# Optimization experiments

Measured on AMD Instinct MI355X. Metric: run time of the kernel, lower is better.

Reference implementation:

```python
import jax, jax.numpy as jnp
import numpy as np

NU, NI, E, NNZ, NLAYERS, TOPK = 2560, 3584, 64, 200000, 2, 5
N = NU + NI
DQK = 4 * E  # Linear(dim, 4*dim)


def setup_inputs() -> dict:
    key = jax.random.key(0)
    ks = jax.random.split(key, 14)
    s = 1.0 / np.sqrt(E)
    return {
        "user_emb": jax.random.normal(ks[0], (NU, E), jnp.float32) * s,
        "item_emb": jax.random.normal(ks[1], (NI, E), jnp.float32) * s,
        "norm_rows": jax.random.randint(ks[2], (NNZ,), 0, N, jnp.int32),
        "norm_cols": jax.random.randint(ks[3], (NNZ,), 0, N, jnp.int32),
        "norm_vals": jax.random.uniform(ks[4], (NNZ,), jnp.float32) / 32.0,
        "adj_rows": jax.random.randint(ks[5], (NNZ,), 0, N, jnp.int32),
        "adj_cols": jax.random.randint(ks[6], (NNZ,), 0, N, jnp.int32),
        "adj_vals": jnp.ones((NNZ,), jnp.float32),
        "Wq": jax.random.normal(ks[7], (DQK, E), jnp.float32) * s,
        "bq": jnp.zeros((DQK,), jnp.float32),
        "Wk": jax.random.normal(ks[8], (DQK, E), jnp.float32) * s,
        "bk": jnp.zeros((DQK,), jnp.float32),
        "Wv": jax.random.normal(ks[9], (DQK, E), jnp.float32) * s,
        "bv": jnp.zeros((DQK,), jnp.float32),
    }


def reference(user_emb, item_emb, norm_rows, norm_cols, norm_vals,
              adj_rows, adj_cols, adj_vals, Wq, bq, Wk, bk, Wv, bv):
    # densified sparse adjacencies (duplicates accumulated, as COO spmm would)
    A_norm = jnp.zeros((N, N), jnp.float32).at[norm_rows, norm_cols].add(norm_vals)
    A = jnp.zeros((N, N), jnp.float32).at[adj_rows, adj_cols].add(adj_vals)

    ego = jnp.concatenate([user_emb, item_emb], axis=0)  # [N, E]
    layers = []
    att_out = None
    for _ in range(NLAYERS):
        layers.append(ego)
        # GNN propagation: sparse.mm(norm_adj, ego)
        ego = A_norm @ ego  # [N, E]
        # dense similarity + sparse-blended similarity
        sim = ego @ ego.T                      # [N, N]
        sim = sim + 0.5 * (A @ sim)            # [N, N]
        # top-K neighbor selection + gather
        _, idx = jax.lax.top_k(sim, TOPK)      # [N, K]
        sample = ego[idx]                      # [N, K, E]
        # SampleAttention: Linear(dim, 4*dim) Q/K/V, scaled dot-product over K neighbors
        q = ego @ Wq.T + bq                    # [N, 4E]
        kk = sample @ Wk.T + bk                # [N, K, 4E]
        vv = sample @ Wv.T + bv                # [N, K, 4E]
        scores = jnp.einsum('nd,nkd->nk', q, kk) / jnp.sqrt(jnp.float32(DQK))
        att = jax.nn.softmax(scores, axis=-1)
        att_out = jnp.einsum('nk,nkd->nd', att, vv)  # [N, 4E]
    mean_emb = jnp.mean(jnp.stack(layers, axis=1), axis=1)  # [N, E]
    return mean_emb[:NU], mean_emb[NU:], att_out
```

## Files before the change

### kernel.cpp

```cpp
#include <hip/hip_runtime.h>
#include <hip/hip_bf16.h>
#include <math.h>

#define NUSER 2560
#define NITEM 3584
#define NN    6144
#define EDIM  64
#define NNZ   200000
#define DQK   256
#define KTOP  5
#define SPLITS 16
#define TPS    3
#define CK     8
#define ELLW   96
#define TPB   256
#define NBUILD 1563
#define BSTR  72

typedef __attribute__((ext_vector_type(8))) short bf16x8;
typedef __attribute__((ext_vector_type(4))) float f32x4;

__device__ __forceinline__ int pack2(float a, float b) {
    __hip_bfloat162 h = __float22bfloat162_rn(float2{a, b});
    return *(int*)&h;
}
__device__ __forceinline__ void ell_unpack(long long v, int* col, float* w) {
    *col = (int)(v & 0xffffffffLL);
    *w   = __int_as_float((int)(v >> 32));
}

__global__ void build_kernel(const int* __restrict__ nr, const int* __restrict__ nc,
                             const float* __restrict__ nv,
                             const int* __restrict__ ar, const int* __restrict__ ac,
                             const float* __restrict__ Wq, const float* __restrict__ Wk,
                             const float* __restrict__ bq,
                             int* __restrict__ cnt_n, int* __restrict__ cnt_a,
                             long long* __restrict__ cv_n, int* __restrict__ cv_a,
                             float* __restrict__ Gbuf) {
    int t = threadIdx.x;

    if (blockIdx.x >= NBUILD) {
        int gb = blockIdx.x - NBUILD;
        if (gb < 16) {
            int ei = gb * 4 + (t >> 6);
            int f  = t & 63;
            float a8[8];
#pragma unroll
            for (int u = 0; u < 8; ++u) a8[u] = 0.f;
            for (int d0 = 0; d0 < DQK; d0 += 8) {
#pragma unroll
                for (int u = 0; u < 8; ++u)
                    a8[u] = fmaf(Wq[(d0 + u) * 64 + ei], Wk[(d0 + u) * 64 + f], a8[u]);
            }
            Gbuf[ei * 64 + f] = ((a8[0] + a8[1]) + (a8[2] + a8[3]))
                              + ((a8[4] + a8[5]) + (a8[6] + a8[7]));
        } else {
            __shared__ float sm[256];
            int f = t & 63, dq = t >> 6;
            float p = 0.f;
            for (int d = dq * 64; d < dq * 64 + 64; ++d)
                p = fmaf(bq[d], Wk[d * 64 + f], p);
            sm[t] = p;
            __syncthreads();
            if (t < 64) Gbuf[4096 + t] = ((sm[t] + sm[64 + t]) + (sm[128 + t] + sm[192 + t]));
        }
        return;
    }

    int g = blockIdx.x * TPB + t;
    if (g < NNZ) {
        int r = nr[g], c = nc[g];
        float v = nv[g];
        int slot = atomicAdd(&cnt_n[r], 1);
        long long pk = (unsigned int)c | ((long long)(unsigned int)__float_as_int(v) << 32);
        cv_n[r * ELLW + slot] = pk;
    } else if (g < 2 * NNZ) {
        int h = g - NNZ;
        int r = ar[h], c = ac[h];
        int slot = atomicAdd(&cnt_a[r], 1);
        cv_a[r * ELLW + slot] = c;
    }
}

__global__ __launch_bounds__(TPB) void spmm_ell_emb_kernel(
        const int* __restrict__ cnt, const long long* __restrict__ cv,
        const float* __restrict__ user, const float* __restrict__ item,
        float* __restrict__ dst) {
    int r = blockIdx.x * 4 + (threadIdx.x >> 6);
    int lane = threadIdx.x & 63;
    int s = r * ELLW, e = s + cnt[r];
    float a[8];
#pragma unroll
    for (int u = 0; u < 8; ++u) a[u] = 0.f;
    int j = s, n8 = s + ((e - s) & ~7);
    for (; j < n8; j += 8) {
        int col[8]; float w[8];
#pragma unroll
        for (int u = 0; u < 8; ++u) ell_unpack(cv[j + u], &col[u], &w[u]);
#pragma unroll
        for (int u = 0; u < 8; ++u) {
            float x = (col[u] < NUSER) ? user[col[u] * EDIM + lane]
                                       : item[(col[u] - NUSER) * EDIM + lane];
            a[u] = fmaf(w[u], x, a[u]);
        }
    }
    for (; j < e; ++j) {
        int col; float w;
        ell_unpack(cv[j], &col, &w);
        float x = (col < NUSER) ? user[col * EDIM + lane] : item[(col - NUSER) * EDIM + lane];
        a[0] = fmaf(w, x, a[0]);
    }
    dst[r * EDIM + lane] = ((a[0] + a[1]) + (a[2] + a[3])) + ((a[4] + a[5]) + (a[6] + a[7]));
}

__global__ __launch_bounds__(TPB) void spmm_ell_kernel(
        const int* __restrict__ cnt, const long long* __restrict__ cv,
        const float* __restrict__ src, float* __restrict__ dst) {
    int r = blockIdx.x * 4 + (threadIdx.x >> 6);
    int lane = threadIdx.x & 63;
    int s = r * ELLW, e = s + cnt[r];
    float a[8];
#pragma unroll
    for (int u = 0; u < 8; ++u) a[u] = 0.f;
    int j = s, n8 = s + ((e - s) & ~7);
    for (; j < n8; j += 8) {
        int col[8]; float w[8];
#pragma unroll
        for (int u = 0; u < 8; ++u) ell_unpack(cv[j + u], &col[u], &w[u]);
#pragma unroll
        for (int u = 0; u < 8; ++u)
            a[u] = fmaf(w[u], src[col[u] * EDIM + lane], a[u]);
    }
    for (; j < e; ++j) {
        int col; float w;
        ell_unpack(cv[j], &col, &w);
        a[0] = fmaf(w, src[col * EDIM + lane], a[0]);
    }
    dst[r * EDIM + lane] = ((a[0] + a[1]) + (a[2] + a[3])) + ((a[4] + a[5]) + (a[6] + a[7]));
}

__global__ __launch_bounds__(TPB) void qm_mean_kernel(
        const int* __restrict__ cnt, const int* __restrict__ cv,
        const float* __restrict__ ego2, const float* __restrict__ ego1,
        const float* __restrict__ user, const float* __restrict__ item,
        float* __restrict__ Qm, float* __restrict__ outmean) {
    int t = threadIdx.x;
    int r = blockIdx.x * 4 + (t >> 6);
    int lane = t & 63;
    int s = r * ELLW, e = s + cnt[r];
    float a[8];
#pragma unroll
    for (int u = 0; u < 8; ++u) a[u] = 0.f;
    int j = s, n8 = s + ((e - s) & ~7);
    for (; j < n8; j += 8) {
        int col[8];
#pragma unroll
        for (int u = 0; u < 8; ++u) col[u] = cv[j + u];
#pragma unroll
        for (int u = 0; u < 8; ++u)
            a[u] += ego2[col[u] * EDIM + lane];
    }
    for (; j < e; ++j) a[0] += ego2[cv[j] * EDIM + lane];
    float acc = ((a[0] + a[1]) + (a[2] + a[3])) + ((a[4] + a[5]) + (a[6] + a[7]));
    int o = r * EDIM + lane;
    Qm[o] = ego2[o] + 0.5f * acc;
    float e0v = (r < NUSER) ? user[o] : item[o - NUSER * EDIM];
    outmean[o] = 0.5f * (e0v + ego1[o]);
}

__device__ __forceinline__ void ins3(float v, int ci, float tv[3], int ti[3]) {
    if (v > tv[2]) {
        bool p1 = v > tv[1], p0 = v > tv[0];
        tv[2] = p1 ? tv[1] : v;  ti[2] = p1 ? ti[1] : ci;
        if (p1) { tv[1] = p0 ? tv[0] : v; ti[1] = p0 ? ti[0] : ci; }
        if (p0) { tv[0] = v; ti[0] = ci; }
    }
}

__global__ __launch_bounds__(TPB, 6) void topk_kernel(
        const float* __restrict__ ego2, const float* __restrict__ Qm,
        int* __restrict__ pidx) {
    __shared__ __align__(16) short smem[13312];
    int t = threadIdx.x;
    int rb = blockIdx.x % 96, sp = blockIdx.x / 96;
    int r0 = rb * 64;
    int w = t >> 6, lane = t & 63, lq = lane >> 4, lc = lane & 15;

    short* Ah = smem;
    short* Bh = smem + 4096;

    {
        int row = t >> 2, seg = t & 3;
        const float4* src = (const float4*)&Qm[(size_t)(r0 + row) * EDIM + seg * 16];
        float4 f0 = src[0], f1 = src[1], f2 = src[2], f3 = src[3];
        int4 p0, p1;
        p0.x = pack2(f0.x, f0.y); p0.y = pack2(f0.z, f0.w);
        p0.z = pack2(f1.x, f1.y); p0.w = pack2(f1.z, f1.w);
        p1.x = pack2(f2.x, f2.y); p1.y = pack2(f2.z, f2.w);
        p1.z = pack2(f3.x, f3.y); p1.w = pack2(f3.z, f3.w);
        *(int4*)&Ah[row * EDIM + seg * 16] = p0;
        *(int4*)&Ah[row * EDIM + seg * 16 + 8] = p1;
    }

    float4 pa[4], pb[4];
    {
        int c0 = (sp * TPS) * 128;
#pragma unroll
        for (int rep = 0; rep < 4; ++rep) {
            int v = t + 256 * rep;
            const float4* src = (const float4*)&ego2[(size_t)(c0 + (v >> 3)) * EDIM + (v & 7) * 8];
            pa[rep] = src[0]; pb[rep] = src[1];
        }
    }

    float t3v[4][3]; int t3i[4][3];
#pragma unroll
    for (int i = 0; i < 4; ++i)
#pragma unroll
        for (int k = 0; k < 3; ++k) { t3v[i][k] = -INFINITY; t3i[i][k] = 0x7fffffff; }

    bf16x8 af0, af1;
    for (int tile = 0; tile < TPS; ++tile) {
        int c0 = (sp * TPS + tile) * 128;
        __syncthreads();
        {
#pragma unroll
            for (int rep = 0; rep < 4; ++rep) {
                int v = t + 256 * rep;
                int4 q;
                q.x = pack2(pa[rep].x, pa[rep].y); q.y = pack2(pa[rep].z, pa[rep].w);
                q.z = pack2(pb[rep].x, pb[rep].y); q.w = pack2(pb[rep].z, pb[rep].w);
                *(int4*)&Bh[(v >> 3) * BSTR + (v & 7) * 8] = q;
            }
        }
        if (tile + 1 < TPS) {
            int c1 = c0 + 128;
#pragma unroll
            for (int rep = 0; rep < 4; ++rep) {
                int v = t + 256 * rep;
                const float4* src = (const float4*)&ego2[(size_t)(c1 + (v >> 3)) * EDIM + (v & 7) * 8];
                pa[rep] = src[0]; pb[rep] = src[1];
            }
        }
        __syncthreads();
        if (tile == 0) {
            af0 = *(const bf16x8*)&Ah[(w * 16 + lc) * EDIM + lq * 8];
            af1 = *(const bf16x8*)&Ah[(w * 16 + lc) * EDIM + 32 + lq * 8];
        }

#pragma unroll
        for (int ch = 0; ch < 8; ++ch) {
            bf16x8 b0 = *(const bf16x8*)&Bh[(ch * 16 + lc) * BSTR + lq * 8];
            bf16x8 b1 = *(const bf16x8*)&Bh[(ch * 16 + lc) * BSTR + 32 + lq * 8];
            f32x4 acc = {0.f, 0.f, 0.f, 0.f};
            acc = __builtin_amdgcn_mfma_f32_16x16x32_bf16(af0, b0, acc, 0, 0, 0);
            acc = __builtin_amdgcn_mfma_f32_16x16x32_bf16(af1, b1, acc, 0, 0, 0);
            int ci = c0 + ch * 16 + lc;
#pragma unroll
            for (int reg = 0; reg < 4; ++reg)
                ins3(acc[reg], ci, t3v[reg], t3i[reg]);
        }
    }

#pragma unroll
    for (int i = 0; i < 4; ++i) {
        int row = r0 + w * 16 + lq * 4 + i;
        float h0 = t3v[i][0], h1 = t3v[i][1], h2 = t3v[i][2];
        int   j0 = t3i[i][0], j1 = t3i[i][1], j2 = t3i[i][2];
        for (int k = 0; k < CK; ++k) {
            float bv = h0; int bi = j0;
#pragma unroll
            for (int off = 1; off < 16; off <<= 1) {
                float ov = __shfl_xor(bv, off, 64);
                int   oi = __shfl_xor(bi, off, 64);
                if (ov > bv || (ov == bv && oi < bi)) { bv = ov; bi = oi; }
            }
            bool cons = (bv == h0 && bi == j0);
            if (cons) { h0 = h1; j0 = j1; h1 = h2; j1 = j2; h2 = -INFINITY; j2 = 0x7fffffff; }
            if (lc == 0) pidx[(row * SPLITS + sp) * CK + k] = bi;
        }
    }
}

__global__ __launch_bounds__(TPB) void attn_sel_kernel(
        const float* __restrict__ Qm, const float* __restrict__ ego2,
        const int* __restrict__ pidx, const float* __restrict__ Gbuf,
        const float* __restrict__ Wv, const float* __restrict__ bv_,
        float* __restrict__ out) {
    __shared__ float sb[4][128];
    __shared__ float sa[4][128];
    __shared__ float smm[4][64];
    __shared__ float sqp[4][64];
    __shared__ float stage[64 * 130];
    int wv = threadIdx.x >> 6, lane = threadIdx.x & 63;
    int t = threadIdx.x;
    int r = blockIdx.x * 4 + wv;
    int ci0 = pidx[r * 128 + lane];
    int ci1 = pidx[r * 128 + 64 + lane];
    int part = lane & 3;

    {
#pragma unroll
        for (int i = 0; i < 17; ++i) {
            int v = i * 256 + t;
            if (v < 4160) stage[v] = Gbuf[v];
        }
    }
    __syncthreads();

    {
        float qv = ego2[(size_t)r * EDIM + lane];
        float pr = stage[4096 + lane];
#pragma unroll 8
        for (int e = 0; e < 64; ++e)
            pr = fmaf(__shfl(qv, e, 64), stage[e * 64 + lane], pr);
        sqp[wv][lane] = pr;
    }

    const float4* qmp = (const float4*)(Qm + (size_t)r * EDIM + part * 16);
    float4 q0 = qmp[0], q1 = qmp[1], q2 = qmp[2], q3 = qmp[3];
    const float4* pmp = (const float4*)&sqp[wv][part * 16];
    float4 p0 = pmp[0], p1 = pmp[1], p2 = pmp[2], p3 = pmp[3];

#pragma unroll
    for (int p = 0; p < 8; ++p) {
        int j = p * 16 + (lane >> 2);
        int c = (j < 64) ? __shfl(ci0, j, 64) : __shfl(ci1, j - 64, 64);
        const float4* ep = (const float4*)(ego2 + (size_t)c * EDIM + part * 16);
        float4 e0 = ep[0], e1 = ep[1], e2 = ep[2], e3 = ep[3];
        float s = 0.f, s2 = 0.f;
        s = fmaf(q0.x, e0.x, s); s = fmaf(q0.y, e0.y, s); s = fmaf(q0.z, e0.z, s); s = fmaf(q0.w, e0.w, s);
        s = fmaf(q1.x, e1.x, s); s = fmaf(q1.y, e1.y, s); s = fmaf(q1.z, e1.z, s); s = fmaf(q1.w, e1.w, s);
        s = fmaf(q2.x, e2.x, s); s = fmaf(q2.y, e2.y, s); s = fmaf(q2.z, e2.z, s); s = fmaf(q2.w, e2.w, s);
        s = fmaf(q3.x, e3.x, s); s = fmaf(q3.y, e3.y, s); s = fmaf(q3.z, e3.z, s); s = fmaf(q3.w, e3.w, s);
        s2 = fmaf(p0.x, e0.x, s2); s2 = fmaf(p0.y, e0.y, s2); s2 = fmaf(p0.z, e0.z, s2); s2 = fmaf(p0.w, e0.w, s2);
        s2 = fmaf(p1.x, e1.x, s2); s2 = fmaf(p1.y, e1.y, s2); s2 = fmaf(p1.z, e1.z, s2); s2 = fmaf(p1.w, e1.w, s2);
        s2 = fmaf(p2.x, e2.x, s2); s2 = fmaf(p2.y, e2.y, s2); s2 = fmaf(p2.z, e2.z, s2); s2 = fmaf(p2.w, e2.w, s2);
        s2 = fmaf(p3.x, e3.x, s2); s2 = fmaf(p3.y, e3.y, s2); s2 = fmaf(p3.z, e3.z, s2); s2 = fmaf(p3.w, e3.w, s2);
        s  += __shfl_xor(s, 1, 64);  s  += __shfl_xor(s, 2, 64);
        s2 += __shfl_xor(s2, 1, 64); s2 += __shfl_xor(s2, 2, 64);
        if (part == 0) { sb[wv][j] = s; sa[wv][j] = s2; }
    }
    float sv0 = sb[wv][lane],      av0 = sa[wv][lane];
    float sv1 = sb[wv][64 + lane], av1 = sa[wv][64 + lane];

    float prevv = INFINITY; int previ = -1;
    int cI[KTOP]; float atk[KTOP];
#pragma unroll
    for (int k = 0; k < KTOP; ++k) {
        bool adm0 = (sv0 < prevv) || (sv0 == prevv && ci0 > previ);
        bool adm1 = (sv1 < prevv) || (sv1 == prevv && ci1 > previ);
        float bv = adm0 ? sv0 : -INFINITY;
        int   bi = adm0 ? ci0 : 0x7fffffff;
        float ba = av0;
        if (adm1 && (sv1 > bv || (sv1 == bv && ci1 < bi))) { bv = sv1; bi = ci1; ba = av1; }
#pragma unroll
        for (int off = 1; off < 64; off <<= 1) {
            float ov = __shfl_xor(bv, off, 64);
            int   oi = __shfl_xor(bi, off, 64);
            float oa = __shfl_xor(ba, off, 64);
            if (ov > bv || (ov == bv && oi < bi)) { bv = ov; bi = oi; ba = oa; }
        }
        cI[k] = bi; atk[k] = ba; prevv = bv; previ = bi;
    }

    float sc[KTOP];
#pragma unroll
    for (int k = 0; k < KTOP; ++k) sc[k] = atk[k] * 0.0625f;
    float mx = sc[0];
#pragma unroll
    for (int k = 1; k < KTOP; ++k) mx = fmaxf(mx, sc[k]);
    float wgt[KTOP], ssum = 0.f;
#pragma unroll
    for (int k = 0; k < KTOP; ++k) { wgt[k] = expf(sc[k] - mx); ssum += wgt[k]; }
    float inv = 1.f / ssum;

    float mm = 0.f;
#pragma unroll
    for (int k = 0; k < KTOP; ++k)
        mm = fmaf(wgt[k] * inv, ego2[(size_t)cI[k] * EDIM + lane], mm);
    smm[wv][lane] = mm;

    int dl = lane * 2;
#pragma unroll
    for (int pass = 0; pass < 2; ++pass) {
        __syncthreads();
#pragma unroll
        for (int i = 0; i < 8; ++i) {
            int idx = i * 256 + t;
            int d  = idx >> 4;
            int e4 = (idx & 15) * 4;
            float4 wv4 = *(const float4*)&Wv[(size_t)(pass * 128 + d) * EDIM + e4];
            stage[(e4 + 0) * 130 + d] = wv4.x;
            stage[(e4 + 1) * 130 + d] = wv4.y;
            stage[(e4 + 2) * 130 + d] = wv4.z;
            stage[(e4 + 3) * 130 + d] = wv4.w;
        }
        __syncthreads();
        float2 acc = *(const float2*)&bv_[pass * 128 + dl];
#pragma unroll 8
        for (int e = 0; e < 64; ++e) {
            float me = smm[wv][e];
            float2 wv2 = *(const float2*)&stage[e * 130 + dl];
            acc.x = fmaf(me, wv2.x, acc.x);
            acc.y = fmaf(me, wv2.y, acc.y);
        }
        *(float2*)&out[(size_t)r * DQK + pass * 128 + dl] = acc;
    }
}

extern "C" void kernel_launch(void* const* d_in, const int* in_sizes, int n_in,
                              void* d_out, int out_size, void* d_ws, size_t ws_size,
                              hipStream_t stream) {
    const float* user  = (const float*)d_in[0];
    const float* item  = (const float*)d_in[1];
    const int*   nrows = (const int*)d_in[2];
    const int*   ncols = (const int*)d_in[3];
    const float* nvals = (const float*)d_in[4];
    const int*   arows = (const int*)d_in[5];
    const int*   acols = (const int*)d_in[6];
    const float* Wq = (const float*)d_in[8];  const float* bq = (const float*)d_in[9];
    const float* Wk = (const float*)d_in[10];
    const float* Wv = (const float*)d_in[12]; const float* bvp = (const float*)d_in[13];
    float* out = (float*)d_out;
    float* ws  = (float*)d_ws;

    const int NE = NN * EDIM;
    float* ego1 = ws;
    float* ego2 = ws + NE;
    float* Qm   = ws + 2 * NE;
    int*   pidx = (int*)(ws + 3 * NE);
    float* Gbuf = ws + 5 * NE;
    int*   ell  = (int*)(ws + 5 * NE + 4160);
    int* cnt_n  = ell;
    int* cnt_a  = ell + 6144;
    long long* cv_n = (long long*)(ell + 12288);
    int* cv_a   = (int*)(cv_n + NN * ELLW);

    hipMemsetAsync(cnt_n, 0, 12288 * sizeof(int), stream);
    build_kernel<<<NBUILD + 17, TPB, 0, stream>>>(nrows, ncols, nvals, arows, acols,
                                                  Wq, Wk, bq,
                                                  cnt_n, cnt_a, cv_n, cv_a, Gbuf);
    spmm_ell_emb_kernel<<<NN / 4, TPB, 0, stream>>>(cnt_n, cv_n, user, item, ego1);
    spmm_ell_kernel<<<NN / 4, TPB, 0, stream>>>(cnt_n, cv_n, ego1, ego2);
    qm_mean_kernel<<<NN / 4, TPB, 0, stream>>>(cnt_a, cv_a, ego2, ego1, user, item, Qm, out);
    topk_kernel<<<96 * SPLITS, TPB, 0, stream>>>(ego2, Qm, pidx);
    attn_sel_kernel<<<NN / 4, TPB, 0, stream>>>(Qm, ego2, pidx, Gbuf, Wv, bvp, out + NE);
}
```

Baseline: 221.7 us.

## Split V projection out of attention kernel into a tiled register-blocked GEMM

The attention-selection kernel no longer restages all of Wv into shared memory in every 4-row block to apply the value projection. It now writes the softmax-weighted neighbor mixture to a workspace buffer, and a separate 64x128-tiled GEMM kernel applies Wv and the bias with 4x8 register blocking. This removes the per-block redundant Wv reload and the extra barriers, and shrinks the attention kernel's shared memory, which may raise occupancy. The cost is one more kernel launch and a round trip of the N x 64 mixture through global memory.

```diff
diff --git a/kernel.cpp b/kernel.cpp
--- a/kernel.cpp
+++ b/kernel.cpp
@@ -285,13 +285,11 @@
 __global__ __launch_bounds__(TPB) void attn_sel_kernel(
         const float* __restrict__ Qm, const float* __restrict__ ego2,
         const int* __restrict__ pidx, const float* __restrict__ Gbuf,
-        const float* __restrict__ Wv, const float* __restrict__ bv_,
-        float* __restrict__ out) {
+        float* __restrict__ m) {
     __shared__ float sb[4][128];
     __shared__ float sa[4][128];
-    __shared__ float smm[4][64];
     __shared__ float sqp[4][64];
-    __shared__ float stage[64 * 130];
+    __shared__ float Gs[4160];
     int wv = threadIdx.x >> 6, lane = threadIdx.x & 63;
     int t = threadIdx.x;
     int r = blockIdx.x * 4 + wv;
@@ -303,17 +301,17 @@
 #pragma unroll
         for (int i = 0; i < 17; ++i) {
             int v = i * 256 + t;
-            if (v < 4160) stage[v] = Gbuf[v];
+            if (v < 4160) Gs[v] = Gbuf[v];
         }
     }
     __syncthreads();
 
     {
         float qv = ego2[(size_t)r * EDIM + lane];
-        float pr = stage[4096 + lane];
+        float pr = Gs[4096 + lane];
 #pragma unroll 8
         for (int e = 0; e < 64; ++e)
-            pr = fmaf(__shfl(qv, e, 64), stage[e * 64 + lane], pr);
+            pr = fmaf(__shfl(qv, e, 64), Gs[e * 64 + lane], pr);
         sqp[wv][lane] = pr;
     }
 
@@ -379,33 +377,72 @@
 #pragma unroll
     for (int k = 0; k < KTOP; ++k)
         mm = fmaf(wgt[k] * inv, ego2[(size_t)cI[k] * EDIM + lane], mm);
-    smm[wv][lane] = mm;
-
-    int dl = lane * 2;
-#pragma unroll
-    for (int pass = 0; pass < 2; ++pass) {
-        __syncthreads();
-#pragma unroll
-        for (int i = 0; i < 8; ++i) {
-            int idx = i * 256 + t;
-            int d  = idx >> 4;
-            int e4 = (idx & 15) * 4;
-            float4 wv4 = *(const float4*)&Wv[(size_t)(pass * 128 + d) * EDIM + e4];
-            stage[(e4 + 0) * 130 + d] = wv4.x;
-            stage[(e4 + 1) * 130 + d] = wv4.y;
-            stage[(e4 + 2) * 130 + d] = wv4.z;
-            stage[(e4 + 3) * 130 + d] = wv4.w;
-        }
-        __syncthreads();
-        float2 acc = *(const float2*)&bv_[pass * 128 + dl];
-#pragma unroll 8
-        for (int e = 0; e < 64; ++e) {
-            float me = smm[wv][e];
-            float2 wv2 = *(const float2*)&stage[e * 130 + dl];
-            acc.x = fmaf(me, wv2.x, acc.x);
-            acc.y = fmaf(me, wv2.y, acc.y);
-        }
-        *(float2*)&out[(size_t)r * DQK + pass * 128 + dl] = acc;
+    m[(size_t)r * EDIM + lane] = mm;
+}
+
+__global__ __launch_bounds__(TPB, 3) void gemm_kernel(
+        const float* __restrict__ A, const float* __restrict__ W,
+        const float* __restrict__ b, float* __restrict__ out) {
+    __shared__ __align__(16) float smem[64 * 64 + 128 * 64];
+    float* As = smem;
+    float* Bs = smem + 4096;
+    int t = threadIdx.x, tx = t & 15, ty = t >> 4;
+    int r0 = blockIdx.x * 64, d0 = blockIdx.y * 128;
+    {
+        int r = t & 63, eb = (t >> 6) * 16;
+#pragma unroll
+        for (int rep = 0; rep < 4; ++rep) {
+            int e0 = eb + rep * 4;
+            float4 v = *(const float4*)&A[(r0 + r) * EDIM + e0];
+            As[(e0 + 0) * 64 + r] = v.x; As[(e0 + 1) * 64 + r] = v.y;
+            As[(e0 + 2) * 64 + r] = v.z; As[(e0 + 3) * 64 + r] = v.w;
+        }
+    }
+    {
+        int d = t & 127, eb = (t >> 7) * 32;
+#pragma unroll
+        for (int rep = 0; rep < 8; ++rep) {
+            int e0 = eb + rep * 4;
+            float4 v = *(const float4*)&W[(d0 + d) * EDIM + e0];
+            Bs[(e0 + 0) * 128 + d] = v.x; Bs[(e0 + 1) * 128 + d] = v.y;
+            Bs[(e0 + 2) * 128 + d] = v.z; Bs[(e0 + 3) * 128 + d] = v.w;
+        }
+    }
+    __syncthreads();
+    float acc[4][8];
+#pragma unroll
+    for (int i = 0; i < 4; ++i)
+#pragma unroll
+        for (int j = 0; j < 8; ++j) acc[i][j] = 0.f;
+#pragma unroll 4
+    for (int e = 0; e < 64; ++e) {
+        float4 a  = *(const float4*)&As[e * 64 + ty * 4];
+        float4 b0 = *(const float4*)&Bs[e * 128 + tx * 4];
+        float4 b1 = *(const float4*)&Bs[e * 128 + 64 + tx * 4];
+        float ar[4] = {a.x, a.y, a.z, a.w};
+#pragma unroll
+        for (int i = 0; i < 4; ++i) {
+            acc[i][0] = fmaf(ar[i], b0.x, acc[i][0]);
+            acc[i][1] = fmaf(ar[i], b0.y, acc[i][1]);
+            acc[i][2] = fmaf(ar[i], b0.z, acc[i][2]);
+            acc[i][3] = fmaf(ar[i], b0.w, acc[i][3]);
+            acc[i][4] = fmaf(ar[i], b1.x, acc[i][4]);
+            acc[i][5] = fmaf(ar[i], b1.y, acc[i][5]);
+            acc[i][6] = fmaf(ar[i], b1.z, acc[i][6]);
+            acc[i][7] = fmaf(ar[i], b1.w, acc[i][7]);
+        }
+    }
+    float4 bias0 = *(const float4*)&b[d0 + tx * 4];
+    float4 bias1 = *(const float4*)&b[d0 + 64 + tx * 4];
+#pragma unroll
+    for (int i = 0; i < 4; ++i) {
+        int r = r0 + ty * 4 + i;
+        float4 o0 = make_float4(acc[i][0] + bias0.x, acc[i][1] + bias0.y,
+                                acc[i][2] + bias0.z, acc[i][3] + bias0.w);
+        float4 o1 = make_float4(acc[i][4] + bias1.x, acc[i][5] + bias1.y,
+                                acc[i][6] + bias1.z, acc[i][7] + bias1.w);
+        *(float4*)&out[r * DQK + d0 + tx * 4] = o0;
+        *(float4*)&out[r * DQK + d0 + 64 + tx * 4] = o1;
     }
 }
 
@@ -430,8 +467,9 @@
     float* ego2 = ws + NE;
     float* Qm   = ws + 2 * NE;
     int*   pidx = (int*)(ws + 3 * NE);
-    float* Gbuf = ws + 5 * NE;
-    int*   ell  = (int*)(ws + 5 * NE + 4160);
+    float* m    = ws + 5 * NE;
+    float* Gbuf = ws + 6 * NE;
+    int*   ell  = (int*)(ws + 6 * NE + 4160);
     int* cnt_n  = ell;
     int* cnt_a  = ell + 6144;
     long long* cv_n = (long long*)(ell + 12288);
@@ -445,5 +483,6 @@
     spmm_ell_kernel<<<NN / 4, TPB, 0, stream>>>(cnt_n, cv_n, ego1, ego2);
     qm_mean_kernel<<<NN / 4, TPB, 0, stream>>>(cnt_a, cv_a, ego2, ego1, user, item, Qm, out);
     topk_kernel<<<96 * SPLITS, TPB, 0, stream>>>(ego2, Qm, pidx);
-    attn_sel_kernel<<<NN / 4, TPB, 0, stream>>>(Qm, ego2, pidx, Gbuf, Wv, bvp, out + NE);
-}
+    attn_sel_kernel<<<NN / 4, TPB, 0, stream>>>(Qm, ego2, pidx, Gbuf, m);
+    gemm_kernel<<<dim3(NN / 64, DQK / 128), TPB, 0, stream>>>(m, Wv, bvp, out + NE);
+}
```

Result: faster. 210.6 us (-5.0%).
